# Kernel tuning notes

Hardware: AMD Instinct MI355X
Metric: run time of the kernel (lower is better)

Reference implementation:

```python
import jax, jax.numpy as jnp
import numpy as np

EMBED_DIM = 1024


def setup_inputs() -> dict:
    key = jax.random.key(0)
    ks = jax.random.split(key, 9)
    d = EMBED_DIM
    s = 1.0 / np.sqrt(d)
    x = jax.random.normal(ks[0], (4, 4096, d), dtype=jnp.float32)
    Wq = jax.random.normal(ks[1], (d, d), dtype=jnp.float32) * s
    bq = jax.random.normal(ks[2], (d,), dtype=jnp.float32) * 0.01
    Wk = jax.random.normal(ks[3], (d, d), dtype=jnp.float32) * s
    bk = jax.random.normal(ks[4], (d,), dtype=jnp.float32) * 0.01
    Wv = jax.random.normal(ks[5], (d, d), dtype=jnp.float32) * s
    bv = jax.random.normal(ks[6], (d,), dtype=jnp.float32) * 0.01
    Wo = jax.random.normal(ks[7], (d, d), dtype=jnp.float32) * s
    bo = jax.random.normal(ks[8], (d,), dtype=jnp.float32) * 0.01
    return {"x": x, "Wq": Wq, "bq": bq, "Wk": Wk, "bk": bk,
            "Wv": Wv, "bv": bv, "Wo": Wo, "bo": bo}


def reference(x, Wq, bq, Wk, bk, Wv, bv, Wo, bo):
    # x: [b, s, d]; single-head attention, scale = 1/sqrt(d)
    b, s, d = x.shape
    q = x @ Wq + bq
    k = x @ Wk + bk
    v = x @ Wv + bv
    scale = 1.0 / jnp.sqrt(jnp.asarray(d, x.dtype))
    scores = jnp.einsum('bqd,bkd->bqk', q, k) * scale  # [b, s, s]
    causal = jnp.tril(jnp.ones((s, s), dtype=bool))
    scores = jnp.where(causal, scores, jnp.asarray(-jnp.inf, scores.dtype))
    attn = jax.nn.softmax(scores, axis=-1)
    ctx = jnp.einsum('bqk,bkd->bqd', attn, v)
    return ctx @ Wo + bo
```

## Files before the change

kernel.cpp:

```cpp
#include <hip/hip_runtime.h>


typedef unsigned short u16;
typedef __attribute__((ext_vector_type(4))) unsigned short u16x4;
typedef __attribute__((ext_vector_type(8))) unsigned short u16x8;
typedef __attribute__((ext_vector_type(8))) __bf16 bf16x8;
typedef __attribute__((ext_vector_type(4))) float f32x4;

typedef const __attribute__((address_space(1))) void* as1cp;
typedef __attribute__((address_space(3))) void* as3p;

#define SBAR() __builtin_amdgcn_s_barrier()
#define SPIN() __builtin_amdgcn_sched_barrier(0)

struct GemmPtrs {
  const u16* A[4];
  const u16* B[4];
  const float* bias[4];
  void* C[4];
};
struct TransPtrs {
  const void* in[4];
  u16* out[4];
};
struct SmPtrs {
  u16* P[4];
};

__device__ __forceinline__ u16 f2bf(float f) {
  union { float f; unsigned int i; } c; c.f = f;
  unsigned int r = c.i + 0x7fffu + ((c.i >> 16) & 1u);
  return (u16)(r >> 16);
}
__device__ __forceinline__ float bf2f(u16 u) {
  union { unsigned int i; float f; } c; c.i = ((unsigned int)u) << 16;
  return c.f;
}

__global__ __launch_bounds__(256) void cast_f32_bf16(const float* __restrict__ in,
                                                     u16* __restrict__ out, int n4) {
  int i = blockIdx.x * blockDim.x + threadIdx.x;
  if (i >= n4) return;
  float4 v = ((const float4*)in)[i];
  u16x4 u;
  u.x = f2bf(v.x); u.y = f2bf(v.y); u.z = f2bf(v.z); u.w = f2bf(v.w);
  ((u16x4*)out)[i] = u;
}

template <bool IN_F32>
__global__ __launch_bounds__(256) void transpose_to_bf16(TransPtrs tp, int R, int C) {
  __shared__ u16 t[32][34];
  int z = blockIdx.z;
  int tx = threadIdx.x, ty = threadIdx.y;
  int c0 = blockIdx.x * 32, r0 = blockIdx.y * 32;
#pragma unroll
  for (int dy = 0; dy < 4; ++dy) {
    int r = r0 + ty + dy * 8;
    int c = c0 + tx;
    u16 hv;
    if (IN_F32) hv = f2bf(((const float*)tp.in[z])[(size_t)r * C + c]);
    else        hv = ((const u16*)tp.in[z])[(size_t)r * C + c];
    t[ty + dy * 8][tx] = hv;
  }
  __syncthreads();
  u16* op = tp.out[z];
#pragma unroll
  for (int dy = 0; dy < 4; ++dy) {
    int a = ty + dy * 8;
    op[(size_t)(c0 + a) * R + r0 + tx] = t[tx][a];
  }
}

__global__ __launch_bounds__(256) void softmax_causal(SmPtrs sp) {
  int row = blockIdx.x;
  u16* P = sp.P[blockIdx.y];
  int tid = threadIdx.x;
  int lane = tid & 63, wv = tid >> 6;
  u16x8* prow = (u16x8*)(P + (size_t)row * 4096);
  int nch = (row >> 3) + 1;
  int fend = ((row >> 7) + 1) << 4;
  int c0 = tid, c1 = tid + 256;
  bool a0 = c0 < nch, a1 = c1 < nch;
  float vals[16];
  float lmax = -3.0e38f;
  if (a0) {
    u16x8 u = prow[c0];
#pragma unroll
    for (int e = 0; e < 8; ++e) {
      float f = (c0 * 8 + e <= row) ? bf2f(u[e]) : -3.0e38f;
      vals[e] = f; lmax = fmaxf(lmax, f);
    }
  } else {
#pragma unroll
    for (int e = 0; e < 8; ++e) vals[e] = -3.0e38f;
  }
  if (a1) {
    u16x8 u = prow[c1];
#pragma unroll
    for (int e = 0; e < 8; ++e) {
      float f = (c1 * 8 + e <= row) ? bf2f(u[e]) : -3.0e38f;
      vals[8 + e] = f; lmax = fmaxf(lmax, f);
    }
  } else {
#pragma unroll
    for (int e = 0; e < 8; ++e) vals[8 + e] = -3.0e38f;
  }
  __shared__ float red[8];
#pragma unroll
  for (int off = 32; off > 0; off >>= 1) lmax = fmaxf(lmax, __shfl_down(lmax, off, 64));
  if (lane == 0) red[wv] = lmax;
  __syncthreads();
  float m2 = fmaxf(fmaxf(red[0], red[1]), fmaxf(red[2], red[3]));
  float lsum = 0.f;
#pragma unroll
  for (int e = 0; e < 16; ++e) {
    float ev = __expf(vals[e] - m2);
    vals[e] = ev;
    lsum += ev;
  }
#pragma unroll
  for (int off = 32; off > 0; off >>= 1) lsum += __shfl_down(lsum, off, 64);
  if (lane == 0) red[4 + wv] = lsum;
  __syncthreads();
  float inv = 1.0f / (red[4] + red[5] + red[6] + red[7]);
  if (a0) {
    u16x8 u;
#pragma unroll
    for (int e = 0; e < 8; ++e) u[e] = f2bf(vals[e] * inv);
    prow[c0] = u;
  }
  if (a1) {
    u16x8 u;
#pragma unroll
    for (int e = 0; e < 8; ++e) u[e] = f2bf(vals[8 + e] * inv);
    prow[c1] = u;
  }
  u16x8 zz = (u16x8)(u16)0;
  for (int c = nch + tid; c < fend; c += 256) prow[c] = zz;
}

template <int MODE, bool OUT_BF16, bool HAS_BIAS>
__global__ __launch_bounds__(512, 2) void gemm256q(GemmPtrs p, int N, float cscale) {
  __shared__ __align__(16) u16 As[2][16384];
  __shared__ __align__(16) u16 Bs[2][16384];
  const int b = blockIdx.x;
  const int tid = threadIdx.x, lane = tid & 63, wv = tid >> 6;
  const int wm = (wv >> 2) << 7, wn = (wv & 3) << 6;
  const int lrow = lane & 15, lquad = lane >> 4;
  const int xsw = lrow & 7;
  const int ch0 = (lquad ^ xsw) << 3;
  const int ch1 = ((4 + lquad) ^ xsw) << 3;
  const int arow = (wm + lrow) * 64;
  const int brow = (wn + lrow) * 64;
  const int soff = (tid >> 3) * 1024 + (((tid & 7) ^ ((tid >> 3) & 7)) << 3);
  const int x = b & 7, u = b >> 3;
  const int nslot = (MODE == 1) ? (u < 4 ? 3 : 2) : (MODE == 0 ? 3 : 1);

  struct TP { const u16* A; const u16* B; int tm, tn, z; };
  auto tileOf = [&](int s) {
    TP t;
    if (MODE == 0) {
      int i = x * 32 + u;
      t.z = s; t.tm = (i >> 2) << 8; t.tn = (i & 3) << 8;
    } else if (MODE == 1) {
      int g = x * 68 + s * 32 + u;
      t.z = g / 136; int L = g - t.z * 136;
      int i = (int)((__fsqrt_rn(8.f * (float)L + 1.f) - 1.f) * 0.5f);
      while ((i + 1) * (i + 2) / 2 <= L) ++i;
      while (i * (i + 1) / 2 > L) --i;
      t.tm = i << 8; t.tn = (L - ((i * (i + 1)) >> 1)) << 8;
    } else {
      int i = x * 32 + u;
      t.z = 0; t.tm = (i >> 2) << 8; t.tn = (i & 3) << 8;
    }
    t.A = p.A[t.z] + (size_t)t.tm * 1024;
    t.B = p.B[t.z] + (size_t)t.tn * 1024;
    return t;
  };

  const u16* gA; const u16* gB; int stk = 0, sslot = 0;
  {
    TP t0 = tileOf(0);
    gA = t0.A + soff; gB = t0.B + soff;
  }
  auto adv = [&]() {
    gA += 64; gB += 64;
    if (++stk == 16) {
      stk = 0;
      if (++sslot < nslot) {
        TP t = tileOf(sslot);
        gA = t.A + soff; gB = t.B + soff;
      }
    }
  };
  auto stage = [&](int sb) __attribute__((always_inline)) {
#pragma unroll
    for (int L = 0; L < 4; ++L)
      __builtin_amdgcn_global_load_lds((as1cp)(gA + L * 65536),
                                       (as3p)(As[sb] + (tid + L * 512) * 8), 16, 0, 0);
#pragma unroll
    for (int L = 0; L < 4; ++L)
      __builtin_amdgcn_global_load_lds((as1cp)(gB + L * 65536),
                                       (as3p)(Bs[sb] + (tid + L * 512) * 8), 16, 0, 0);
    adv();
  };

  f32x4 acc[8][4];
#pragma unroll
  for (int i = 0; i < 8; ++i)
#pragma unroll
    for (int j = 0; j < 4; ++j) acc[i][j] = (f32x4){0.f, 0.f, 0.f, 0.f};

  auto epi = [&](int cs2) {
    TP t = tileOf(cs2);
    float bvv[4] = {0.f, 0.f, 0.f, 0.f};
    if constexpr (HAS_BIAS) {
#pragma unroll
      for (int n = 0; n < 4; ++n) bvv[n] = p.bias[t.z][t.tn + wn + n * 16 + lrow];
    }
#pragma unroll
    for (int m = 0; m < 8; ++m)
#pragma unroll
      for (int r = 0; r < 4; ++r) {
        size_t row = (size_t)(t.tm + wm + m * 16 + lquad * 4 + r);
#pragma unroll
        for (int n = 0; n < 4; ++n) {
          int col = t.tn + wn + n * 16 + lrow;
          float vvv = acc[m][n][r] * cscale + bvv[n];
          if (OUT_BF16) ((u16*)p.C[t.z])[row * N + col] = f2bf(vvv);
          else          ((float*)p.C[t.z])[row * N + col] = vvv;
        }
      }
#pragma unroll
    for (int m2 = 0; m2 < 8; ++m2)
#pragma unroll
      for (int n2 = 0; n2 < 4; ++n2) acc[m2][n2] = (f32x4){0.f, 0.f, 0.f, 0.f};
  };

  stage(0);
  asm volatile("s_waitcnt vmcnt(0)");
  SBAR();
  SPIN();

  const int T = nslot * 16;
  int cs = 0;
  for (int t = 0; t < T; ++t) {
    const int cb = t & 1;
    if (t + 1 < T) {
      stage(cb ^ 1);
      SPIN();
      asm volatile("s_waitcnt vmcnt(8)");
    } else {
      SPIN();
      asm volatile("s_waitcnt vmcnt(0)");
    }
    SBAR();
    SPIN();
    __builtin_amdgcn_s_setprio(1);
    {
      bf16x8 af[4], bf[4];
#pragma unroll
      for (int m = 0; m < 4; ++m) af[m] = *(const bf16x8*)&As[cb][arow + m * 1024 + ch0];
#pragma unroll
      for (int n = 0; n < 4; ++n) bf[n] = *(const bf16x8*)&Bs[cb][brow + n * 1024 + ch0];
#pragma unroll
      for (int m = 0; m < 4; ++m)
#pragma unroll
        for (int n = 0; n < 4; ++n)
          acc[m][n] = __builtin_amdgcn_mfma_f32_16x16x32_bf16(af[m], bf[n], acc[m][n], 0, 0, 0);
#pragma unroll
      for (int m = 0; m < 4; ++m) af[m] = *(const bf16x8*)&As[cb][arow + 4096 + m * 1024 + ch0];
#pragma unroll
      for (int m = 0; m < 4; ++m)
#pragma unroll
        for (int n = 0; n < 4; ++n)
          acc[4 + m][n] = __builtin_amdgcn_mfma_f32_16x16x32_bf16(af[m], bf[n], acc[4 + m][n], 0, 0, 0);
#pragma unroll
      for (int m = 0; m < 4; ++m) af[m] = *(const bf16x8*)&As[cb][arow + 4096 + m * 1024 + ch1];
#pragma unroll
      for (int n = 0; n < 4; ++n) bf[n] = *(const bf16x8*)&Bs[cb][brow + n * 1024 + ch1];
#pragma unroll
      for (int m = 0; m < 4; ++m)
#pragma unroll
        for (int n = 0; n < 4; ++n)
          acc[4 + m][n] = __builtin_amdgcn_mfma_f32_16x16x32_bf16(af[m], bf[n], acc[4 + m][n], 0, 0, 0);
#pragma unroll
      for (int m = 0; m < 4; ++m) af[m] = *(const bf16x8*)&As[cb][arow + m * 1024 + ch1];
#pragma unroll
      for (int m = 0; m < 4; ++m)
#pragma unroll
        for (int n = 0; n < 4; ++n)
          acc[m][n] = __builtin_amdgcn_mfma_f32_16x16x32_bf16(af[m], bf[n], acc[m][n], 0, 0, 0);
    }
    __builtin_amdgcn_s_setprio(0);
    SBAR();
    SPIN();
    if (((t + 1) & 15) == 0) { epi(cs); ++cs; }
  }
}

__global__ __launch_bounds__(512, 2) void gemm_pv64(GemmPtrs p) {
  __shared__ __align__(16) u16 As[2][8192];
  __shared__ __align__(16) u16 Bs[2][16384];
  const int b = blockIdx.x;
  const int tid = threadIdx.x, lane = tid & 63, wv = tid >> 6;
  const int wm = (wv >> 2) << 6, wn = (wv & 3) << 6;
  const int lrow = lane & 15, lquad = lane >> 4;
  const int xsw = lrow & 7;
  const int ch0 = (lquad ^ xsw) << 3;
  const int ch1 = ((4 + lquad) ^ xsw) << 3;
  const int arow = (wm + lrow) * 64;
  const int brow = (wn + lrow) * 64;
  const int soff = (tid >> 3) * 4096 + (((tid & 7) ^ ((tid >> 3) & 7)) << 3);
  const int x = b & 7, u = b >> 3;
  const int P = x * 32 + u;
  const int z = P >> 6, j = (P >> 2) & 15, n4 = P & 3;
  const int i1 = j, i2 = 31 - j;
  const int tn = n4 << 8;
  const int T1 = 2 * (i1 + 1);
  const int T = 66;
  const u16* Abase = p.A[z];
  const u16* Bbase = p.B[z] + (size_t)tn * 4096;

  const u16* gA = Abase + (size_t)(i1 << 7) * 4096 + soff;
  const u16* gB = Bbase + soff;
  int stk = 0;
  auto adv = [&]() {
    gA += 64; gB += 64;
    if (++stk == T1) {
      gA = Abase + (size_t)(i2 << 7) * 4096 + soff;
      gB = Bbase + soff;
    }
  };
  auto stage = [&](int sb) __attribute__((always_inline)) {
#pragma unroll
    for (int L = 0; L < 2; ++L)
      __builtin_amdgcn_global_load_lds((as1cp)(gA + (size_t)L * 262144),
                                       (as3p)(As[sb] + (tid + L * 512) * 8), 16, 0, 0);
#pragma unroll
    for (int L = 0; L < 4; ++L)
      __builtin_amdgcn_global_load_lds((as1cp)(gB + (size_t)L * 262144),
                                       (as3p)(Bs[sb] + (tid + L * 512) * 8), 16, 0, 0);
    adv();
  };

  f32x4 acc[4][4];
#pragma unroll
  for (int i = 0; i < 4; ++i)
#pragma unroll
    for (int jj = 0; jj < 4; ++jj) acc[i][jj] = (f32x4){0.f, 0.f, 0.f, 0.f};

  auto epi = [&](int s) {
    int tm = (s ? i2 : i1) << 7;
#pragma unroll
    for (int m = 0; m < 4; ++m)
#pragma unroll
      for (int r = 0; r < 4; ++r) {
        size_t row = (size_t)(tm + wm + m * 16 + lquad * 4 + r);
#pragma unroll
        for (int n = 0; n < 4; ++n) {
          int col = tn + wn + n * 16 + lrow;
          ((u16*)p.C[z])[row * 1024 + col] = f2bf(acc[m][n][r]);
        }
      }
#pragma unroll
    for (int m2 = 0; m2 < 4; ++m2)
#pragma unroll
      for (int n2 = 0; n2 < 4; ++n2) acc[m2][n2] = (f32x4){0.f, 0.f, 0.f, 0.f};
  };

  stage(0);
  asm volatile("s_waitcnt vmcnt(0)");
  SBAR();
  SPIN();

  for (int t = 0; t < T; ++t) {
    const int cb = t & 1;
    if (t + 1 < T) {
      stage(cb ^ 1);
      SPIN();
      asm volatile("s_waitcnt vmcnt(6)");
    } else {
      SPIN();
      asm volatile("s_waitcnt vmcnt(0)");
    }
    SBAR();
    SPIN();
    __builtin_amdgcn_s_setprio(1);
    {
      bf16x8 af[4], bf[4];
#pragma unroll
      for (int m = 0; m < 4; ++m) af[m] = *(const bf16x8*)&As[cb][arow + m * 1024 + ch0];
#pragma unroll
      for (int n = 0; n < 4; ++n) bf[n] = *(const bf16x8*)&Bs[cb][brow + n * 1024 + ch0];
#pragma unroll
      for (int m = 0; m < 4; ++m)
#pragma unroll
        for (int n = 0; n < 4; ++n)
          acc[m][n] = __builtin_amdgcn_mfma_f32_16x16x32_bf16(af[m], bf[n], acc[m][n], 0, 0, 0);
#pragma unroll
      for (int m = 0; m < 4; ++m) af[m] = *(const bf16x8*)&As[cb][arow + m * 1024 + ch1];
#pragma unroll
      for (int n = 0; n < 4; ++n) bf[n] = *(const bf16x8*)&Bs[cb][brow + n * 1024 + ch1];
#pragma unroll
      for (int m = 0; m < 4; ++m)
#pragma unroll
        for (int n = 0; n < 4; ++n)
          acc[m][n] = __builtin_amdgcn_mfma_f32_16x16x32_bf16(af[m], bf[n], acc[m][n], 0, 0, 0);
    }
    __builtin_amdgcn_s_setprio(0);
    SBAR();
    SPIN();
    if (t + 1 == T1) epi(0);
  }
  epi(1);
}

extern "C" void kernel_launch(void* const* d_in, const int* in_sizes, int n_in,
                              void* d_out, int out_size, void* d_ws, size_t ws_size,
                              hipStream_t stream) {
  const float* x  = (const float*)d_in[0];
  const float* Wq = (const float*)d_in[1];
  const float* bq = (const float*)d_in[2];
  const float* Wk = (const float*)d_in[3];
  const float* bk = (const float*)d_in[4];
  const float* Wv = (const float*)d_in[5];
  const float* bv = (const float*)d_in[6];
  const float* Wo = (const float*)d_in[7];
  const float* bo = (const float*)d_in[8];

  const int S = 4096, D = 1024;
  const size_t XE = (size_t)4 * S * D;
  const size_t BSE = (size_t)S * D;

  char* ws = (char*)d_ws;
  u16* xb  = (u16*)(ws + 0);
  u16* q   = (u16*)(ws + 33554432);
  u16* k   = (u16*)(ws + 67108864);
  u16* v   = (u16*)(ws + 100663296);
  u16* ctx = (u16*)(ws + 134217728);
  u16* wqT = (u16*)(ws + 167772160);
  u16* wkT = wqT + 1048576;
  u16* wvT = wkT + 1048576;
  u16* woT = wvT + 1048576;
  u16* attn2 = (u16*)(ws + 176160768);
  u16* attn0 = (u16*)d_out;
  u16* attn1 = attn0 + (size_t)S * S;
  u16* attn3 = v;
  u16* vT = xb;
  u16* attn[4] = {attn0, attn1, attn2, attn3};

  cast_f32_bf16<<<(int)(XE / 4 / 256), 256, 0, stream>>>(x, xb, (int)(XE / 4));
  {
    TransPtrs tp = {{Wq, Wk, Wv, Wo}, {wqT, wkT, wvT, woT}};
    transpose_to_bf16<true><<<dim3(32, 32, 4), dim3(32, 8), 0, stream>>>(tp, D, D);
  }
  {
    GemmPtrs gp = {{xb, xb, xb, xb}, {wqT, wkT, wvT, wqT},
                   {bq, bk, bv, bq}, {q, k, v, q}};
    gemm256q<0, true, true><<<256, 512, 0, stream>>>(gp, D, 1.0f);
  }
  {
    TransPtrs tp = {{v, v + BSE, v + 2 * BSE, v + 3 * BSE},
                    {vT, vT + BSE, vT + 2 * BSE, vT + 3 * BSE}};
    transpose_to_bf16<false><<<dim3(D / 32, S / 32, 4), dim3(32, 8), 0, stream>>>(tp, S, D);
  }
  {
    GemmPtrs gp = {{q, q + BSE, q + 2 * BSE, q + 3 * BSE},
                   {k, k + BSE, k + 2 * BSE, k + 3 * BSE},
                   {nullptr, nullptr, nullptr, nullptr},
                   {attn[0], attn[1], attn[2], attn[3]}};
    gemm256q<1, true, false><<<256, 512, 0, stream>>>(gp, S, 0.03125f);
  }
  {
    SmPtrs sp = {{attn[0], attn[1], attn[2], attn[3]}};
    softmax_causal<<<dim3(S, 4), 256, 0, stream>>>(sp);
  }
  {
    GemmPtrs gp = {{attn[0], attn[1], attn[2], attn[3]},
                   {vT, vT + BSE, vT + 2 * BSE, vT + 3 * BSE},
                   {nullptr, nullptr, nullptr, nullptr},
                   {ctx, ctx + BSE, ctx + 2 * BSE, ctx + 3 * BSE}};
    gemm_pv64<<<256, 512, 0, stream>>>(gp);
  }
  {
    GemmPtrs gp = {{ctx, ctx, ctx, ctx}, {woT, woT, woT, woT},
                   {bo, bo, bo, bo}, {d_out, d_out, d_out, d_out}};
    gemm256q<3, false, true><<<256, 512, 0, stream>>>(gp, D, 1.0f);
  }
}
```

Before: 518.7 us.

## Switch GEMMs to triple-buffered K=32 pipeline with split A/B staging phases

Replaces the double-buffered K=64 LDS pipeline in both GEMM kernels with a triple-buffered K=32 pipeline. Each iteration loads fragments and issues the next-next stage's global->LDS loads, interleaved across two half-phases with barriers. The aim is to overlap global loads with MFMA more finely and halve LDS per buffer. The cost is more barriers and iterations per tile, plus a new swizzle layout for the 32-wide rows.

Result: faster. 508.3 us (-2.0%).

```diff
diff --git a/kernel.cpp b/kernel.cpp
--- a/kernel.cpp
+++ b/kernel.cpp
@@ -140,19 +140,17 @@
 }
 
 template <int MODE, bool OUT_BF16, bool HAS_BIAS>
-__global__ __launch_bounds__(512, 2) void gemm256q(GemmPtrs p, int N, float cscale) {
-  __shared__ __align__(16) u16 As[2][16384];
-  __shared__ __align__(16) u16 Bs[2][16384];
+__global__ __launch_bounds__(512, 2) void gemm8ph(GemmPtrs p, int N, float cscale) {
+  __shared__ __align__(16) u16 As[3][8192];
+  __shared__ __align__(16) u16 Bs[3][8192];
   const int b = blockIdx.x;
   const int tid = threadIdx.x, lane = tid & 63, wv = tid >> 6;
   const int wm = (wv >> 2) << 7, wn = (wv & 3) << 6;
   const int lrow = lane & 15, lquad = lane >> 4;
-  const int xsw = lrow & 7;
-  const int ch0 = (lquad ^ xsw) << 3;
-  const int ch1 = ((4 + lquad) ^ xsw) << 3;
-  const int arow = (wm + lrow) * 64;
-  const int brow = (wn + lrow) * 64;
-  const int soff = (tid >> 3) * 1024 + (((tid & 7) ^ ((tid >> 3) & 7)) << 3);
+  const int xs = (lquad ^ ((lrow >> 1) & 3)) << 3;
+  const int aoff0 = (wm + lrow) * 32 + xs;
+  const int boff0 = (wn + lrow) * 32 + xs;
+  const int soff = (tid >> 2) * 1024 + (((tid & 3) ^ ((tid >> 3) & 3)) << 3);
   const int x = b & 7, u = b >> 3;
   const int nslot = (MODE == 1) ? (u < 4 ? 3 : 2) : (MODE == 0 ? 3 : 1);
 
@@ -184,8 +182,8 @@
     gA = t0.A + soff; gB = t0.B + soff;
   }
   auto adv = [&]() {
-    gA += 64; gB += 64;
-    if (++stk == 16) {
+    gA += 32; gB += 32;
+    if (++stk == 32) {
       stk = 0;
       if (++sslot < nslot) {
         TP t = tileOf(sslot);
@@ -193,15 +191,13 @@
       }
     }
   };
-  auto stage = [&](int sb) __attribute__((always_inline)) {
-#pragma unroll
-    for (int L = 0; L < 4; ++L)
-      __builtin_amdgcn_global_load_lds((as1cp)(gA + L * 65536),
-                                       (as3p)(As[sb] + (tid + L * 512) * 8), 16, 0, 0);
-#pragma unroll
-    for (int L = 0; L < 4; ++L)
-      __builtin_amdgcn_global_load_lds((as1cp)(gB + L * 65536),
-                                       (as3p)(Bs[sb] + (tid + L * 512) * 8), 16, 0, 0);
+  auto stgA = [&](int s) __attribute__((always_inline)) {
+    __builtin_amdgcn_global_load_lds((as1cp)gA, (as3p)(As[s] + wv * 512), 16, 0, 0);
+    __builtin_amdgcn_global_load_lds((as1cp)(gA + 131072), (as3p)(As[s] + 4096 + wv * 512), 16, 0, 0);
+  };
+  auto stgB = [&](int s) __attribute__((always_inline)) {
+    __builtin_amdgcn_global_load_lds((as1cp)gB, (as3p)(Bs[s] + wv * 512), 16, 0, 0);
+    __builtin_amdgcn_global_load_lds((as1cp)(gB + 131072), (as3p)(Bs[s] + 4096 + wv * 512), 16, 0, 0);
     adv();
   };
 
@@ -237,110 +233,98 @@
       for (int n2 = 0; n2 < 4; ++n2) acc[m2][n2] = (f32x4){0.f, 0.f, 0.f, 0.f};
   };
 
-  stage(0);
-  asm volatile("s_waitcnt vmcnt(0)");
+  stgA(0); stgB(0);
+  stgA(1); stgB(1);
+  asm volatile("s_waitcnt vmcnt(4)");
   SBAR();
   SPIN();
 
-  const int T = nslot * 16;
-  int cs = 0;
+  const int T = nslot * 32;
+  int cs = 0, c = 0;
   for (int t = 0; t < T; ++t) {
-    const int cb = t & 1;
-    if (t + 1 < T) {
-      stage(cb ^ 1);
-      SPIN();
-      asm volatile("s_waitcnt vmcnt(8)");
-    } else {
-      SPIN();
-      asm volatile("s_waitcnt vmcnt(0)");
-    }
-    SBAR();
+    const int s = (c >= 1) ? c - 1 : 2;
+    const bool stg = (t + 2) < T;
+    bf16x8 af[4], bf[4];
+#pragma unroll
+    for (int m = 0; m < 4; ++m) af[m] = *(const bf16x8*)&As[c][aoff0 + m * 512];
+#pragma unroll
+    for (int n = 0; n < 4; ++n) bf[n] = *(const bf16x8*)&Bs[c][boff0 + n * 512];
+    if (stg) stgA(s);
+    SPIN();
+    SBAR();
+    asm volatile("s_waitcnt lgkmcnt(0)");
     SPIN();
     __builtin_amdgcn_s_setprio(1);
-    {
-      bf16x8 af[4], bf[4];
-#pragma unroll
-      for (int m = 0; m < 4; ++m) af[m] = *(const bf16x8*)&As[cb][arow + m * 1024 + ch0];
-#pragma unroll
-      for (int n = 0; n < 4; ++n) bf[n] = *(const bf16x8*)&Bs[cb][brow + n * 1024 + ch0];
-#pragma unroll
-      for (int m = 0; m < 4; ++m)
-#pragma unroll
-        for (int n = 0; n < 4; ++n)
-          acc[m][n] = __builtin_amdgcn_mfma_f32_16x16x32_bf16(af[m], bf[n], acc[m][n], 0, 0, 0);
-#pragma unroll
-      for (int m = 0; m < 4; ++m) af[m] = *(const bf16x8*)&As[cb][arow + 4096 + m * 1024 + ch0];
-#pragma unroll
-      for (int m = 0; m < 4; ++m)
-#pragma unroll
-        for (int n = 0; n < 4; ++n)
-          acc[4 + m][n] = __builtin_amdgcn_mfma_f32_16x16x32_bf16(af[m], bf[n], acc[4 + m][n], 0, 0, 0);
-#pragma unroll
-      for (int m = 0; m < 4; ++m) af[m] = *(const bf16x8*)&As[cb][arow + 4096 + m * 1024 + ch1];
-#pragma unroll
-      for (int n = 0; n < 4; ++n) bf[n] = *(const bf16x8*)&Bs[cb][brow + n * 1024 + ch1];
-#pragma unroll
-      for (int m = 0; m < 4; ++m)
-#pragma unroll
-        for (int n = 0; n < 4; ++n)
-          acc[4 + m][n] = __builtin_amdgcn_mfma_f32_16x16x32_bf16(af[m], bf[n], acc[4 + m][n], 0, 0, 0);
-#pragma unroll
-      for (int m = 0; m < 4; ++m) af[m] = *(const bf16x8*)&As[cb][arow + m * 1024 + ch1];
-#pragma unroll
-      for (int m = 0; m < 4; ++m)
-#pragma unroll
-        for (int n = 0; n < 4; ++n)
-          acc[m][n] = __builtin_amdgcn_mfma_f32_16x16x32_bf16(af[m], bf[n], acc[m][n], 0, 0, 0);
-    }
+#pragma unroll
+    for (int m = 0; m < 4; ++m)
+#pragma unroll
+      for (int n = 0; n < 4; ++n)
+        acc[m][n] = __builtin_amdgcn_mfma_f32_16x16x32_bf16(af[m], bf[n], acc[m][n], 0, 0, 0);
     __builtin_amdgcn_s_setprio(0);
-    SBAR();
-    SPIN();
-    if (((t + 1) & 15) == 0) { epi(cs); ++cs; }
-  }
-}
-
-__global__ __launch_bounds__(512, 2) void gemm_pv64(GemmPtrs p) {
-  __shared__ __align__(16) u16 As[2][8192];
-  __shared__ __align__(16) u16 Bs[2][16384];
+    SPIN();
+    SBAR();
+#pragma unroll
+    for (int m = 0; m < 4; ++m) af[m] = *(const bf16x8*)&As[c][aoff0 + 2048 + m * 512];
+    if (stg) stgB(s);
+    SPIN();
+    if (stg)               asm volatile("s_waitcnt vmcnt(4)");
+    else if (t + 1 < T)    asm volatile("s_waitcnt vmcnt(0)");
+    SBAR();
+    asm volatile("s_waitcnt lgkmcnt(0)");
+    SPIN();
+    __builtin_amdgcn_s_setprio(1);
+#pragma unroll
+    for (int m = 0; m < 4; ++m)
+#pragma unroll
+      for (int n = 0; n < 4; ++n)
+        acc[4 + m][n] = __builtin_amdgcn_mfma_f32_16x16x32_bf16(af[m], bf[n], acc[4 + m][n], 0, 0, 0);
+    __builtin_amdgcn_s_setprio(0);
+    SPIN();
+    SBAR();
+    if (((t + 1) & 31) == 0) { SPIN(); epi(cs); ++cs; }
+    if (++c == 3) c = 0;
+  }
+}
+
+__global__ __launch_bounds__(512, 2) void gemm_pv3(GemmPtrs p) {
+  __shared__ __align__(16) u16 As[3][4096];
+  __shared__ __align__(16) u16 Bs[3][8192];
   const int b = blockIdx.x;
   const int tid = threadIdx.x, lane = tid & 63, wv = tid >> 6;
   const int wm = (wv >> 2) << 6, wn = (wv & 3) << 6;
   const int lrow = lane & 15, lquad = lane >> 4;
-  const int xsw = lrow & 7;
-  const int ch0 = (lquad ^ xsw) << 3;
-  const int ch1 = ((4 + lquad) ^ xsw) << 3;
-  const int arow = (wm + lrow) * 64;
-  const int brow = (wn + lrow) * 64;
-  const int soff = (tid >> 3) * 4096 + (((tid & 7) ^ ((tid >> 3) & 7)) << 3);
+  const int xs = (lquad ^ ((lrow >> 1) & 3)) << 3;
+  const int aoff0 = (wm + lrow) * 32 + xs;
+  const int boff0 = (wn + lrow) * 32 + xs;
+  const int soff = (tid >> 2) * 4096 + (((tid & 3) ^ ((tid >> 3) & 3)) << 3);
   const int x = b & 7, u = b >> 3;
   const int P = x * 32 + u;
   const int z = P >> 6, j = (P >> 2) & 15, n4 = P & 3;
   const int i1 = j, i2 = 31 - j;
   const int tn = n4 << 8;
-  const int T1 = 2 * (i1 + 1);
-  const int T = 66;
+  const int T1 = (i1 + 1) * 4;
+  const int niter1 = (i2 + 1) * 4;
   const u16* Abase = p.A[z];
   const u16* Bbase = p.B[z] + (size_t)tn * 4096;
 
   const u16* gA = Abase + (size_t)(i1 << 7) * 4096 + soff;
   const u16* gB = Bbase + soff;
-  int stk = 0;
+  int stk = 0, sslot = 0;
   auto adv = [&]() {
-    gA += 64; gB += 64;
-    if (++stk == T1) {
+    gA += 32; gB += 32;
+    ++stk;
+    if (sslot == 0 && stk == T1) {
+      stk = 0; sslot = 1;
       gA = Abase + (size_t)(i2 << 7) * 4096 + soff;
       gB = Bbase + soff;
-    }
-  };
-  auto stage = [&](int sb) __attribute__((always_inline)) {
-#pragma unroll
-    for (int L = 0; L < 2; ++L)
-      __builtin_amdgcn_global_load_lds((as1cp)(gA + (size_t)L * 262144),
-                                       (as3p)(As[sb] + (tid + L * 512) * 8), 16, 0, 0);
-#pragma unroll
-    for (int L = 0; L < 4; ++L)
-      __builtin_amdgcn_global_load_lds((as1cp)(gB + (size_t)L * 262144),
-                                       (as3p)(Bs[sb] + (tid + L * 512) * 8), 16, 0, 0);
+    } else if (sslot == 1 && stk == niter1) {
+      stk = 0; sslot = 2;
+    }
+  };
+  auto stage = [&](int s) __attribute__((always_inline)) {
+    __builtin_amdgcn_global_load_lds((as1cp)gA, (as3p)(As[s] + wv * 512), 16, 0, 0);
+    __builtin_amdgcn_global_load_lds((as1cp)gB, (as3p)(Bs[s] + wv * 512), 16, 0, 0);
+    __builtin_amdgcn_global_load_lds((as1cp)(gB + 524288), (as3p)(Bs[s] + 4096 + wv * 512), 16, 0, 0);
     adv();
   };
 
@@ -369,49 +353,39 @@
       for (int n2 = 0; n2 < 4; ++n2) acc[m2][n2] = (f32x4){0.f, 0.f, 0.f, 0.f};
   };
 
-  stage(0);
-  asm volatile("s_waitcnt vmcnt(0)");
+  stage(0); stage(1);
+  asm volatile("s_waitcnt vmcnt(3)");
   SBAR();
   SPIN();
 
+  const int T = 132;
+  int c = 0;
   for (int t = 0; t < T; ++t) {
-    const int cb = t & 1;
-    if (t + 1 < T) {
-      stage(cb ^ 1);
-      SPIN();
-      asm volatile("s_waitcnt vmcnt(6)");
-    } else {
-      SPIN();
-      asm volatile("s_waitcnt vmcnt(0)");
-    }
-    SBAR();
+    const int s = (c >= 1) ? c - 1 : 2;
+    const bool stg = (t + 2) < T;
+    bf16x8 af[4], bf[4];
+#pragma unroll
+    for (int m = 0; m < 4; ++m) af[m] = *(const bf16x8*)&As[c][aoff0 + m * 512];
+#pragma unroll
+    for (int n = 0; n < 4; ++n) bf[n] = *(const bf16x8*)&Bs[c][boff0 + n * 512];
+    if (stg) stage(s);
+    SPIN();
+    if (stg)            asm volatile("s_waitcnt vmcnt(3)");
+    else if (t + 1 < T) asm volatile("s_waitcnt vmcnt(0)");
+    SBAR();
+    asm volatile("s_waitcnt lgkmcnt(0)");
     SPIN();
     __builtin_amdgcn_s_setprio(1);
-    {
-      bf16x8 af[4], bf[4];
-#pragma unroll
-      for (int m = 0; m < 4; ++m) af[m] = *(const bf16x8*)&As[cb][arow + m * 1024 + ch0];
-#pragma unroll
-      for (int n = 0; n < 4; ++n) bf[n] = *(const bf16x8*)&Bs[cb][brow + n * 1024 + ch0];
-#pragma unroll
-      for (int m = 0; m < 4; ++m)
-#pragma unroll
-        for (int n = 0; n < 4; ++n)
-          acc[m][n] = __builtin_amdgcn_mfma_f32_16x16x32_bf16(af[m], bf[n], acc[m][n], 0, 0, 0);
-#pragma unroll
-      for (int m = 0; m < 4; ++m) af[m] = *(const bf16x8*)&As[cb][arow + m * 1024 + ch1];
-#pragma unroll
-      for (int n = 0; n < 4; ++n) bf[n] = *(const bf16x8*)&Bs[cb][brow + n * 1024 + ch1];
-#pragma unroll
-      for (int m = 0; m < 4; ++m)
-#pragma unroll
-        for (int n = 0; n < 4; ++n)
-          acc[m][n] = __builtin_amdgcn_mfma_f32_16x16x32_bf16(af[m], bf[n], acc[m][n], 0, 0, 0);
-    }
+#pragma unroll
+    for (int m = 0; m < 4; ++m)
+#pragma unroll
+      for (int n = 0; n < 4; ++n)
+        acc[m][n] = __builtin_amdgcn_mfma_f32_16x16x32_bf16(af[m], bf[n], acc[m][n], 0, 0, 0);
     __builtin_amdgcn_s_setprio(0);
-    SBAR();
-    SPIN();
-    if (t + 1 == T1) epi(0);
+    SPIN();
+    SBAR();
+    if (t + 1 == T1) { SPIN(); epi(0); }
+    if (++c == 3) c = 0;
   }
   epi(1);
 }
@@ -458,7 +432,7 @@
   {
     GemmPtrs gp = {{xb, xb, xb, xb}, {wqT, wkT, wvT, wqT},
                    {bq, bk, bv, bq}, {q, k, v, q}};
-    gemm256q<0, true, true><<<256, 512, 0, stream>>>(gp, D, 1.0f);
+    gemm8ph<0, true, true><<<256, 512, 0, stream>>>(gp, D, 1.0f);
   }
   {
     TransPtrs tp = {{v, v + BSE, v + 2 * BSE, v + 3 * BSE},
@@ -470,7 +444,7 @@
                    {k, k + BSE, k + 2 * BSE, k + 3 * BSE},
                    {nullptr, nullptr, nullptr, nullptr},
                    {attn[0], attn[1], attn[2], attn[3]}};
-    gemm256q<1, true, false><<<256, 512, 0, stream>>>(gp, S, 0.03125f);
+    gemm8ph<1, true, false><<<256, 512, 0, stream>>>(gp, S, 0.03125f);
   }
   {
     SmPtrs sp = {{attn[0], attn[1], attn[2], attn[3]}};
@@ -481,11 +455,11 @@
                    {vT, vT + BSE, vT + 2 * BSE, vT + 3 * BSE},
                    {nullptr, nullptr, nullptr, nullptr},
                    {ctx, ctx + BSE, ctx + 2 * BSE, ctx + 3 * BSE}};
-    gemm_pv64<<<256, 512, 0, stream>>>(gp);
+    gemm_pv3<<<256, 512, 0, stream>>>(gp);
   }
   {
     GemmPtrs gp = {{ctx, ctx, ctx, ctx}, {woT, woT, woT, woT},
                    {bo, bo, bo, bo}, {d_out, d_out, d_out, d_out}};
-    gemm256q<3, false, true><<<256, 512, 0, stream>>>(gp, D, 1.0f);
-  }
-}
+    gemm8ph<3, false, true><<<256, 512, 0, stream>>>(gp, D, 1.0f);
+  }
+}
```
